# Performance work log

Measured on AMD Instinct MI355X. Metric: run time of the kernel, lower is better.

Reference implementation:

```python
import jax, jax.numpy as jnp
import numpy as np


def batch_pairwise_dist(x, y):
    # x: (B, Nx, 3), y: (B, Ny, 3) -> P: (B, Nx, Ny) squared euclidean dists
    xx = jnp.sum(x * x, axis=-1)                      # (B, Nx)
    yy = jnp.sum(y * y, axis=-1)                      # (B, Ny)
    zz = jnp.einsum('bnd,bmd->bnm', x, y)             # (B, Nx, Ny)
    return xx[:, :, None] + yy[:, None, :] - 2.0 * zz


def huber(x, c):
    return jnp.where(x < c, 0.5 * x * x, c * x - 0.5 * c * c)


def global_align_loss(preds, gts, c):
    # preds, gts: (B, N, 3) point sets; faithful to GlobalAlignLoss.forward
    P = batch_pairwise_dist(gts, preds)               # (B, Ngt, Npred)
    loss_1 = jnp.sum(huber(jnp.min(P, axis=1), c))
    loss_2 = jnp.sum(huber(jnp.min(P, axis=2), c))
    return loss_1 + loss_2


def setup_inputs() -> dict:
    key = jax.random.key(0)
    ks = jax.random.split(key, 8)
    B, KP, K, N = 4, 512, 32, 4096
    return {
        'src_keypoints': jax.random.normal(ks[0], (B, 3, KP), dtype=jnp.float32),
        'tgt_keypoints': jax.random.normal(ks[1], (B, 3, KP), dtype=jnp.float32),
        'rotation_ab': jax.random.normal(ks[2], (B, 3, 3), dtype=jnp.float32),
        'translation_ab': jax.random.normal(ks[3], (B, 3), dtype=jnp.float32),
        'src_keypoints_knn': jax.random.normal(ks[4], (B, 3, KP, K), dtype=jnp.float32),
        'tgt_keypoints_knn': jax.random.normal(ks[5], (B, 3, KP, K), dtype=jnp.float32),
        'k': K,
        'src_transformed': jax.random.normal(ks[6], (B, 3, N), dtype=jnp.float32),
        'tgt': jax.random.normal(ks[7], (B, 3, N), dtype=jnp.float32),
    }


def reference(src_keypoints, tgt_keypoints, rotation_ab, translation_ab,
              src_keypoints_knn, tgt_keypoints_knn, k, src_transformed, tgt):
    margin = 0.01  # loss_margin from init
    # Global alignment loss on full clouds (points last -> points first)
    gal = global_align_loss(jnp.transpose(src_transformed, (0, 2, 1)),
                            jnp.transpose(tgt, (0, 2, 1)), margin)
    # se3.transform: p' = R @ p + t, applied to keypoints (B, 3, KP)
    transformed_srckps = jnp.einsum('bij,bjn->bin', rotation_ab, src_keypoints) \
        + translation_ab[:, :, None]
    keypoints_loss = jnp.sum((transformed_srckps - tgt_keypoints) ** 2)
    knn_consensus_loss = jnp.sum((src_keypoints_knn - tgt_keypoints_knn) ** 2)
    neighborhood_consensus_loss = knn_consensus_loss / k + keypoints_loss
    return (neighborhood_consensus_loss, gal)
```

## Files before the change

kernel.cpp:

```cpp
#include <hip/hip_runtime.h>

#define NPTS 4096
#define NB   4
#define KP   512
#define HUBER_C 0.01f
#define QCHUNK 128
#define NQC (NPTS / QCHUNK)
#define GAL_BLOCKS (2 * NB * NQC)
#define NPK (NPTS / 2)

typedef float v2f __attribute__((ext_vector_type(2)));



__device__ inline float huber_f(float x) {
    return (x < HUBER_C) ? 0.5f * x * x
                         : fmaf(HUBER_C, x, -0.5f * HUBER_C * HUBER_C);
}

__device__ inline v2f splat2(float s) { v2f r; r.x = s; r.y = s; return r; }


__global__ void init_kernel(float* __restrict__ out) {
    if (threadIdx.x < 2) out[threadIdx.x] = 0.0f;
}

__global__ __launch_bounds__(256) void main_kernel(
    const float* __restrict__ srcT, const float* __restrict__ tgtT,
    const float* __restrict__ skp, const float* __restrict__ tkp,
    const float* __restrict__ R, const float* __restrict__ T,
    const float* __restrict__ aknn, const float* __restrict__ bknn,
    const int* __restrict__ kptr, float* __restrict__ out,
    int knn_blocks, int knn_quads)
{
    __shared__ float4 lds_a[NPK];
    __shared__ float4 lds_b[NPK];
    __shared__ float pmin[QCHUNK];
    __shared__ float red[4];

    const int bid = blockIdx.x;
    const int tid = threadIdx.x;
    const int kp_blocks = (NB * KP) / 256;
    const int pre = knn_blocks + kp_blocks;
    float contrib = 0.0f;
    float* target;

    if (bid >= pre) {
        const int gb  = bid - pre;
        const int qc  = gb & (NQC - 1);
        const int b   = (gb >> 5) & 3;
        const int dir = gb >> 7;
        const float* qb = (dir ? tgtT : srcT) + b * 3 * NPTS;
        const float* ob = (dir ? srcT : tgtT) + b * 3 * NPTS;

        #pragma unroll
        for (int idx = tid; idx < NPK; idx += 256) {
            int j = 2 * idx;
            float2 X = *(const float2*)(ob + j);
            float2 Y = *(const float2*)(ob + NPTS + j);
            float2 Z = *(const float2*)(ob + 2 * NPTS + j);
            float w0 = fmaf(X.x, X.x, fmaf(Y.x, Y.x, Z.x * Z.x));
            float w1 = fmaf(X.y, X.y, fmaf(Y.y, Y.y, Z.y * Z.y));
            lds_a[idx] = make_float4(X.x, X.y, Y.x, Y.y);
            lds_b[idx] = make_float4(Z.x, Z.y, w0, w1);
        }

        const int q = qc * QCHUNK + (tid & (QCHUNK - 1));
        const float qx = qb[q], qy = qb[NPTS + q], qz = qb[2 * NPTS + q];
        const float ax = -2.0f * qx, ay = -2.0f * qy, az = -2.0f * qz;
        const float qw2 = fmaf(qx, qx, fmaf(qy, qy, qz * qz));
        const int h = tid >> 7;
        __syncthreads();

        const float4* la = lds_a + h * (NPK / 2);
        const float4* lb = lds_b + h * (NPK / 2);
        v2f mm; mm.x = 3.0e38f; mm.y = 3.0e38f;
        auto pack_step = [&](const float4& A, const float4& B) -> v2f {
            v2f X, Y, Z, W;
            X.x = A.x; X.y = A.y; Y.x = A.z; Y.y = A.w;
            Z.x = B.x; Z.y = B.y; W.x = B.z; W.y = B.w;
            return __builtin_elementwise_fma(X, splat2(ax),
                   __builtin_elementwise_fma(Y, splat2(ay),
                   __builtin_elementwise_fma(Z, splat2(az), W)));
        };
        #pragma unroll 4
        for (int p = 0; p < NPK / 2; p += 2) {
            v2f t0 = pack_step(la[p],     lb[p]);
            v2f t1 = pack_step(la[p + 1], lb[p + 1]);
            mm.x = fminf(mm.x, fminf(t0.x, t1.x));
            mm.y = fminf(mm.y, fminf(t0.y, t1.y));
        }
        float m = fminf(mm.x, mm.y);
        if (h) pmin[tid & (QCHUNK - 1)] = m;
        __syncthreads();
        if (!h) contrib = huber_f(fminf(m, pmin[tid]) + qw2);
        target = out + 1;
    } else if (bid < knn_blocks) {
        int i = bid * 256 + tid;
        if (i < knn_quads) {
            float4 va = ((const float4*)aknn)[i];
            float4 vb = ((const float4*)bknn)[i];
            float dx = va.x - vb.x, dy = va.y - vb.y;
            float dz = va.z - vb.z, dw = va.w - vb.w;
            contrib = fmaf(dx, dx, fmaf(dy, dy, fmaf(dz, dz, dw * dw)));
        }
        contrib *= 1.0f / (float)(*kptr);
        target = out;
    } else {
        int i = (bid - knn_blocks) * 256 + tid;
        int b = i >> 9;
        int n = i & (KP - 1);
        const float* r = R + b * 9;
        const float* t = T + b * 3;
        const float* s = skp + b * 3 * KP;
        const float* g = tkp + b * 3 * KP;
        float sx = s[n], sy = s[KP + n], sz = s[2 * KP + n];
        #pragma unroll
        for (int d = 0; d < 3; ++d) {
            float v = fmaf(r[d*3+0], sx, fmaf(r[d*3+1], sy, fmaf(r[d*3+2], sz, t[d])))
                      - g[d * KP + n];
            contrib = fmaf(v, v, contrib);
        }
        target = out;
    }

    float v = contrib;
    #pragma unroll
    for (int off = 32; off; off >>= 1) v += __shfl_down(v, off, 64);
    if ((tid & 63) == 0) red[tid >> 6] = v;
    __syncthreads();
    if (tid == 0)
        atomicAdd(target, red[0] + red[1] + red[2] + red[3]);
}


extern "C" void kernel_launch(void* const* d_in, const int* in_sizes, int n_in,
                              void* d_out, int out_size, void* d_ws, size_t ws_size,
                              hipStream_t stream) {
    const float* skp  = (const float*)d_in[0];
    const float* tkp  = (const float*)d_in[1];
    const float* R    = (const float*)d_in[2];
    const float* T    = (const float*)d_in[3];
    const float* aknn = (const float*)d_in[4];
    const float* bknn = (const float*)d_in[5];
    const int*   kptr = (const int*)d_in[6];
    const float* srcT = (const float*)d_in[7];
    const float* tgtT = (const float*)d_in[8];
    float* out = (float*)d_out;

    const int knn_quads  = in_sizes[4] / 4;
    const int knn_blocks = (knn_quads + 255) / 256;
    const int kp_blocks  = (NB * KP + 255) / 256;
    const int total      = knn_blocks + kp_blocks + GAL_BLOCKS;

    init_kernel<<<1, 64, 0, stream>>>(out);
    main_kernel<<<total, 256, 0, stream>>>(
        srcT, tgtT, skp, tkp, R, T, aknn, bknn, kptr, out,
        knn_blocks, knn_quads);
}
```

Before: 95.04 us.

## Register-block 8 queries per thread across 16 point groups in chamfer min

Each thread now holds 8 query points in registers and scans a 1/16 slice of the other cloud. This replaces the old scheme of one query per thread over half the cloud, so each LDS load is reused 8 times. Partial minima go through a padded shared buffer and are reduced over 16 groups. The LDS layout is padded to avoid bank conflicts, and the GAL blocks are moved to the front of the grid so the heavy work is scheduled first. Register pressure rises, which may lower occupancy.

```diff
diff --git a/kernel.cpp b/kernel.cpp
--- a/kernel.cpp
+++ b/kernel.cpp
@@ -8,6 +8,11 @@
 #define NQC (NPTS / QCHUNK)
 #define GAL_BLOCKS (2 * NB * NQC)
 #define NPK (NPTS / 2)
+#define NOG 16
+#define PKG (NPK / NOG)
+#define QPT 8
+#define LDA_STRIDE (PKG + 1)
+#define PMIN_STRIDE (QCHUNK + 4)
 
 typedef float v2f __attribute__((ext_vector_type(2)));
 
@@ -33,70 +38,84 @@
     const int* __restrict__ kptr, float* __restrict__ out,
     int knn_blocks, int knn_quads)
 {
-    __shared__ float4 lds_a[NPK];
-    __shared__ float4 lds_b[NPK];
-    __shared__ float pmin[QCHUNK];
+    __shared__ float4 lds_a[NOG * LDA_STRIDE];
+    __shared__ float4 lds_b[NOG * LDA_STRIDE];
+    __shared__ float pminl[NOG * PMIN_STRIDE];
     __shared__ float red[4];
 
     const int bid = blockIdx.x;
     const int tid = threadIdx.x;
-    const int kp_blocks = (NB * KP) / 256;
-    const int pre = knn_blocks + kp_blocks;
     float contrib = 0.0f;
     float* target;
 
-    if (bid >= pre) {
-        const int gb  = bid - pre;
-        const int qc  = gb & (NQC - 1);
-        const int b   = (gb >> 5) & 3;
-        const int dir = gb >> 7;
+    if (bid < GAL_BLOCKS) {
+        const int qc  = bid & (NQC - 1);
+        const int b   = (bid >> 5) & 3;
+        const int dir = bid >> 7;
         const float* qb = (dir ? tgtT : srcT) + b * 3 * NPTS;
         const float* ob = (dir ? srcT : tgtT) + b * 3 * NPTS;
 
         #pragma unroll
-        for (int idx = tid; idx < NPK; idx += 256) {
+        for (int k = 0; k < NPK / 256; ++k) {
+            int idx = tid + k * 256;
             int j = 2 * idx;
             float2 X = *(const float2*)(ob + j);
             float2 Y = *(const float2*)(ob + NPTS + j);
             float2 Z = *(const float2*)(ob + 2 * NPTS + j);
             float w0 = fmaf(X.x, X.x, fmaf(Y.x, Y.x, Z.x * Z.x));
             float w1 = fmaf(X.y, X.y, fmaf(Y.y, Y.y, Z.y * Z.y));
-            lds_a[idx] = make_float4(X.x, X.y, Y.x, Y.y);
-            lds_b[idx] = make_float4(Z.x, Z.y, w0, w1);
+            int li = idx + (idx >> 7);
+            lds_a[li] = make_float4(X.x, X.y, Y.x, Y.y);
+            lds_b[li] = make_float4(Z.x, Z.y, w0, w1);
         }
 
-        const int q = qc * QCHUNK + (tid & (QCHUNK - 1));
-        const float qx = qb[q], qy = qb[NPTS + q], qz = qb[2 * NPTS + q];
-        const float ax = -2.0f * qx, ay = -2.0f * qy, az = -2.0f * qz;
-        const float qw2 = fmaf(qx, qx, fmaf(qy, qy, qz * qz));
-        const int h = tid >> 7;
+        const int ql0 = tid & 15;
+        const int og  = tid >> 4;
+        float ax[QPT], ay[QPT], az[QPT], qw[QPT];
+        v2f mm[QPT];
+        #pragma unroll
+        for (int j = 0; j < QPT; ++j) {
+            int q = qc * QCHUNK + ql0 + 16 * j;
+            float x = qb[q], y = qb[NPTS + q], z = qb[2 * NPTS + q];
+            ax[j] = -2.0f * x; ay[j] = -2.0f * y; az[j] = -2.0f * z;
+            qw[j] = fmaf(x, x, fmaf(y, y, z * z));
+            mm[j].x = 3.0e38f; mm[j].y = 3.0e38f;
+        }
         __syncthreads();
 
-        const float4* la = lds_a + h * (NPK / 2);
-        const float4* lb = lds_b + h * (NPK / 2);
-        v2f mm; mm.x = 3.0e38f; mm.y = 3.0e38f;
-        auto pack_step = [&](const float4& A, const float4& B) -> v2f {
+        const float4* la = lds_a + og * LDA_STRIDE;
+        const float4* lb = lds_b + og * LDA_STRIDE;
+        #pragma unroll 4
+        for (int p = 0; p < PKG; ++p) {
+            float4 A = la[p], B = lb[p];
             v2f X, Y, Z, W;
             X.x = A.x; X.y = A.y; Y.x = A.z; Y.y = A.w;
             Z.x = B.x; Z.y = B.y; W.x = B.z; W.y = B.w;
-            return __builtin_elementwise_fma(X, splat2(ax),
-                   __builtin_elementwise_fma(Y, splat2(ay),
-                   __builtin_elementwise_fma(Z, splat2(az), W)));
-        };
-        #pragma unroll 4
-        for (int p = 0; p < NPK / 2; p += 2) {
-            v2f t0 = pack_step(la[p],     lb[p]);
-            v2f t1 = pack_step(la[p + 1], lb[p + 1]);
-            mm.x = fminf(mm.x, fminf(t0.x, t1.x));
-            mm.y = fminf(mm.y, fminf(t0.y, t1.y));
+            #pragma unroll
+            for (int j = 0; j < QPT; ++j) {
+                v2f t = __builtin_elementwise_fma(X, splat2(ax[j]),
+                        __builtin_elementwise_fma(Y, splat2(ay[j]),
+                        __builtin_elementwise_fma(Z, splat2(az[j]), W)));
+                mm[j] = __builtin_elementwise_min(mm[j], t);
+            }
         }
-        float m = fminf(mm.x, mm.y);
-        if (h) pmin[tid & (QCHUNK - 1)] = m;
+
+        #pragma unroll
+        for (int j = 0; j < QPT; ++j)
+            pminl[og * PMIN_STRIDE + ql0 + 16 * j] =
+                fminf(mm[j].x, mm[j].y) + qw[j];
         __syncthreads();
-        if (!h) contrib = huber_f(fminf(m, pmin[tid]) + qw2);
+
+        if (tid < QCHUNK) {
+            float m = 3.0e38f;
+            #pragma unroll
+            for (int g = 0; g < NOG; ++g)
+                m = fminf(m, pminl[g * PMIN_STRIDE + tid]);
+            contrib = huber_f(m);
+        }
         target = out + 1;
-    } else if (bid < knn_blocks) {
-        int i = bid * 256 + tid;
+    } else if (bid < GAL_BLOCKS + knn_blocks) {
+        int i = (bid - GAL_BLOCKS) * 256 + tid;
         if (i < knn_quads) {
             float4 va = ((const float4*)aknn)[i];
             float4 vb = ((const float4*)bknn)[i];
@@ -107,7 +126,7 @@
         contrib *= 1.0f / (float)(*kptr);
         target = out;
     } else {
-        int i = (bid - knn_blocks) * 256 + tid;
+        int i = (bid - GAL_BLOCKS - knn_blocks) * 256 + tid;
         int b = i >> 9;
         int n = i & (KP - 1);
         const float* r = R + b * 9;
@@ -151,7 +170,7 @@
     const int knn_quads  = in_sizes[4] / 4;
     const int knn_blocks = (knn_quads + 255) / 256;
     const int kp_blocks  = (NB * KP + 255) / 256;
-    const int total      = knn_blocks + kp_blocks + GAL_BLOCKS;
+    const int total      = GAL_BLOCKS + knn_blocks + kp_blocks;
 
     init_kernel<<<1, 64, 0, stream>>>(out);
     main_kernel<<<total, 256, 0, stream>>>(
```

Result: faster. 86.29 us, median of 2 (-9.2%).
